# Optimization experiments

Hardware: AMD Instinct MI355X
Metric: run time of the kernel (lower is better)

The kernel has to match this reference:

```python
import jax, jax.numpy as jnp
import numpy as np
import math

D_MODEL = 1024
N_HEADS = 16
D_FF = 4096
KERNEL = 25
EPS = 1e-5


def setup_inputs() -> dict:
    key = jax.random.key(0)
    ks = jax.random.split(key, 16)
    B, L, D = 2, 2048, D_MODEL
    s = 0.02
    inp = {
        'x': jax.random.normal(ks[0], (B, L, D), dtype=jnp.float32),
        'Wq': jax.random.normal(ks[1], (D, D), dtype=jnp.float32) * s,
        'bq': jnp.zeros((D,), jnp.float32),
        'Wk': jax.random.normal(ks[2], (D, D), dtype=jnp.float32) * s,
        'bk': jnp.zeros((D,), jnp.float32),
        'Wv': jax.random.normal(ks[3], (D, D), dtype=jnp.float32) * s,
        'bv': jnp.zeros((D,), jnp.float32),
        'Wo': jax.random.normal(ks[4], (D, D), dtype=jnp.float32) * s,
        'bo': jnp.zeros((D,), jnp.float32),
        'W1': jax.random.normal(ks[5], (D_FF, D), dtype=jnp.float32) * s,
        'b1': jnp.zeros((D_FF,), jnp.float32),
        'W2': jax.random.normal(ks[6], (D, D_FF), dtype=jnp.float32) * s,
        'b2': jnp.zeros((D,), jnp.float32),
        'g1': jnp.ones((D,), jnp.float32),
        'be1': jnp.zeros((D,), jnp.float32),
        'g2': jnp.ones((D,), jnp.float32),
        'be2': jnp.zeros((D,), jnp.float32),
    }
    return inp


def moving_avg(x):
    # torch AvgPool1d(kernel=25, stride=1, padding=12, count_include_pad=True)
    # x: (B, L, D) -> trend: (B, L, D)
    pad = KERNEL // 2
    xp = jnp.pad(x, ((0, 0), (pad, pad), (0, 0)))
    c = jnp.cumsum(xp, axis=1)
    c = jnp.concatenate([jnp.zeros_like(c[:, :1]), c], axis=1)
    return (c[:, KERNEL:] - c[:, :-KERNEL]) / KERNEL


def layernorm(x, g, b):
    mu = jnp.mean(x, axis=-1, keepdims=True)
    var = jnp.mean((x - mu) ** 2, axis=-1, keepdims=True)
    return (x - mu) * jax.lax.rsqrt(var + EPS) * g + b


def reference(x, Wq, bq, Wk, bk, Wv, bv, Wo, bo, W1, b1, W2, b2, g1, be1, g2, be2):
    B, L, D = x.shape
    H, dk = N_HEADS, D // N_HEADS
    # projections (torch Linear: y = x @ W.T + b)
    q = (x @ Wq.T + bq).reshape(B, L, H, dk).transpose(0, 2, 1, 3)
    k = (x @ Wk.T + bk).reshape(B, L, H, dk).transpose(0, 2, 1, 3)
    v = (x @ Wv.T + bv).reshape(B, L, H, dk).transpose(0, 2, 1, 3)
    scores = jnp.einsum('bhld,bhmd->bhlm', q, k) / math.sqrt(dk)
    t = jnp.arange(L, dtype=jnp.float32)
    time_bias = -0.1 * jnp.abs(t[None, :] - t[:, None])  # (L, L)
    attn = jax.nn.softmax(scores + time_bias[None, None], axis=-1)
    ao = jnp.einsum('bhlm,bhmd->bhld', attn, v)
    ao = ao.transpose(0, 2, 1, 3).reshape(B, L, D)
    attn_out = ao @ Wo.T + bo
    x = x + attn_out
    x = moving_avg(x)  # trend kept (x, _ = decomp1(x))
    x = layernorm(x, g1, be1)
    ff = jax.nn.gelu(x @ W1.T + b1, approximate=False) @ W2.T + b2
    x = x + ff
    x = moving_avg(x)  # trend kept again
    x = layernorm(x, g2, be2)
    return x
```

## Files before the change

### kernel.cpp

```cpp
#include <hip/hip_runtime.h>
#include <hip/hip_bf16.h>
#include <math.h>

#define DMODEL 1024
#define LSEQ   2048
#define BATCH  2
#define NHEADS 16
#define DHEAD  64
#define DFF    4096
#define MROWS  (BATCH*LSEQ)

typedef __attribute__((ext_vector_type(8))) short short8;
typedef __attribute__((ext_vector_type(4))) float f32x4;
using bf16 = __hip_bfloat16;

static __device__ __forceinline__ f32x4 mfma16(short8 a, short8 b, f32x4 c) {
    return __builtin_amdgcn_mfma_f32_16x16x32_bf16(a, b, c, 0, 0, 0);
}

static __device__ __forceinline__ void gload16(const void* g, void* l) {
    __builtin_amdgcn_global_load_lds(
        (const __attribute__((address_space(1))) char*)g,
        (__attribute__((address_space(3))) char*)l, 16, 0, 0);
}

static __device__ __forceinline__ bf16 b16(float v) { return __float2bfloat16(v); }

__global__ void f2b1_kernel(const float* __restrict__ in, bf16* __restrict__ out, int n4) {
    int i = blockIdx.x * blockDim.x + threadIdx.x;
    if (i >= n4) return;
    float4 v = reinterpret_cast<const float4*>(in)[i];
    union { ushort4 u; bf16 h[4]; } o;
    o.h[0] = b16(v.x); o.h[1] = b16(v.y); o.h[2] = b16(v.z); o.h[3] = b16(v.w);
    reinterpret_cast<ushort4*>(out)[i] = o.u;
}

__global__ void f2b4_kernel(const float* p0, const float* p1, const float* p2, const float* p3,
                            bf16* o0, bf16* o1, bf16* o2, bf16* o3, int n4) {
    const float* in; bf16* out;
    switch (blockIdx.y) {
        case 0: in = p0; out = o0; break;
        case 1: in = p1; out = o1; break;
        case 2: in = p2; out = o2; break;
        default: in = p3; out = o3; break;
    }
    int i = blockIdx.x * blockDim.x + threadIdx.x;
    if (i >= n4) return;
    float4 v = reinterpret_cast<const float4*>(in)[i];
    union { ushort4 u; bf16 h[4]; } o;
    o.h[0] = b16(v.x); o.h[1] = b16(v.y); o.h[2] = b16(v.z); o.h[3] = b16(v.w);
    reinterpret_cast<ushort4*>(out)[i] = o.u;
}

__global__ void concat3_kernel(const float* __restrict__ a, const float* __restrict__ b,
                               const float* __restrict__ c, float* __restrict__ o) {
    int i = blockIdx.x * blockDim.x + threadIdx.x;
    if (i < DMODEL) { o[i] = a[i]; o[DMODEL + i] = b[i]; o[2 * DMODEL + i] = c[i]; }
}

template<int S>
__global__ __launch_bounds__(256) void reduce_kernel(const float* __restrict__ res,
                                                     const float* __restrict__ P,
                                                     const float* __restrict__ bias,
                                                     float* __restrict__ out, int n4) {
    int i = blockIdx.x * blockDim.x + threadIdx.x;
    if (i >= n4) return;
    float4 acc = reinterpret_cast<const float4*>(res)[i];
#pragma unroll
    for (int s = 0; s < S; ++s) {
        float4 p = reinterpret_cast<const float4*>(P)[i + (size_t)s * (MROWS * DMODEL / 4)];
        acc.x += p.x; acc.y += p.y; acc.z += p.z; acc.w += p.w;
    }
    float4 bs = reinterpret_cast<const float4*>(bias)[i & (DMODEL / 4 - 1)];
    acc.x += bs.x; acc.y += bs.y; acc.z += bs.z; acc.w += bs.w;
    reinterpret_cast<float4*>(out)[i] = acc;
}

template<int EPI>
__global__ __launch_bounds__(256) void gemm_bt(const bf16* __restrict__ A,
                                               const bf16* __restrict__ W,
                                               const float* __restrict__ bias,
                                               void* __restrict__ Cout,
                                               int M, int N, int lda, int ldw, int K) {
    __shared__ bf16 sm[16384];
    const int t    = threadIdx.x;
    const int m0   = blockIdx.x * 128;
    const int n0   = blockIdx.y * 128;
    const int sk   = blockIdx.z;
    const int wave = t >> 6, lane = t & 63;
    const int wr   = (wave >> 1) * 64;
    const int wc   = (wave & 1) * 64;
    const int lr   = lane & 15, lkb = lane >> 4;
    const int srow = t >> 2, scol = (t & 3) * 8;

    const bf16* Ag0 = A + (size_t)(m0 + srow) * lda + (size_t)sk * K + scol;
    const bf16* Ag1 = A + (size_t)(m0 + 64 + srow) * lda + (size_t)sk * K + scol;
    const bf16* Wg0 = W + (size_t)(n0 + srow) * ldw + (size_t)sk * K + scol;
    const bf16* Wg1 = W + (size_t)(n0 + 64 + srow) * ldw + (size_t)sk * K + scol;

    f32x4 acc[4][4];
#pragma unroll
    for (int i = 0; i < 4; ++i)
#pragma unroll
        for (int j = 0; j < 4; ++j)
            acc[i][j] = (f32x4){0.f, 0.f, 0.f, 0.f};

    const int nt = K >> 5;
    auto stage = [&](int buf, int kt) {
        const int off = kt * 32;
        bf16* AsW = sm + buf * 4096 + wave * 512;
        bf16* WsW = sm + 8192 + buf * 4096 + wave * 512;
        gload16(Ag0 + off, AsW);
        gload16(Ag1 + off, AsW + 2048);
        gload16(Wg0 + off, WsW);
        gload16(Wg1 + off, WsW + 2048);
    };

    stage(0, 0);
    __syncthreads();
    int cur = 0;
    for (int kt = 0; kt < nt; ++kt) {
        if (kt + 1 < nt) stage(cur ^ 1, kt + 1);
        short8 a[4], b[4];
#pragma unroll
        for (int i = 0; i < 4; ++i)
            a[i] = *reinterpret_cast<const short8*>(
                &sm[cur * 4096 + (wr + i * 16 + lr) * 32 + lkb * 8]);
#pragma unroll
        for (int j = 0; j < 4; ++j)
            b[j] = *reinterpret_cast<const short8*>(
                &sm[8192 + cur * 4096 + (wc + j * 16 + lr) * 32 + lkb * 8]);
#pragma unroll
        for (int i = 0; i < 4; ++i)
#pragma unroll
            for (int j = 0; j < 4; ++j)
                acc[i][j] = mfma16(b[j], a[i], acc[i][j]);
        __syncthreads();
        cur ^= 1;
    }

    float* Cp = (float*)Cout + (EPI == 3 ? (size_t)sk * M * N : 0);
#pragma unroll
    for (int i = 0; i < 4; ++i) {
        const int row = m0 + wr + i * 16 + lr;
#pragma unroll
        for (int j = 0; j < 4; ++j) {
            const int col = n0 + wc + j * 16 + lkb * 4;
            f32x4 v = acc[i][j];
            if (EPI != 3) {
                float4 bs = *reinterpret_cast<const float4*>(&bias[col]);
                v[0] += bs.x; v[1] += bs.y; v[2] += bs.z; v[3] += bs.w;
            }
            if (EPI == 0 || EPI == 3) {
                float4 ov; ov.x = v[0]; ov.y = v[1]; ov.z = v[2]; ov.w = v[3];
                *reinterpret_cast<float4*>(&Cp[(size_t)row * N + col]) = ov;
            } else if (EPI == 1) {
                union { ushort4 u; bf16 h[4]; } ob;
#pragma unroll
                for (int q = 0; q < 4; ++q) {
                    float x = v[q];
                    float u2 = x * (1.5957691216f + 0.0713548162f * x * x);
                    float e = __expf(fminf(u2, 60.f));
                    ob.h[q] = b16(x * (e / (e + 1.f)));
                }
                *reinterpret_cast<ushort4*>(
                    &reinterpret_cast<bf16*>(Cout)[(size_t)row * N + col]) = ob.u;
            } else {
                union { ushort4 u; bf16 h[4]; } ob;
#pragma unroll
                for (int q = 0; q < 4; ++q) ob.h[q] = b16(v[q]);
                *reinterpret_cast<ushort4*>(
                    &reinterpret_cast<bf16*>(Cout)[(size_t)row * N + col]) = ob.u;
            }
        }
    }
}

__global__ __launch_bounds__(256) void attn_kernel(const bf16* __restrict__ Q,
                                                   const bf16* __restrict__ Km,
                                                   const bf16* __restrict__ V,
                                                   bf16* __restrict__ O,
                                                   int ldq, int ldo) {
    __shared__ bf16 Qs[64][72];
    __shared__ bf16 Ks[64][72];
    __shared__ bf16 VsT[64][72];
    __shared__ bf16 Ps[64][72];
    const int t    = threadIdx.x;
    const int wave = t >> 6, lane = t & 63;
    const int lr   = lane & 15, lkb = lane >> 4;
    const int qt   = blockIdx.x;
    const int q0   = qt * 64;
    const int b    = blockIdx.y >> 4, h = blockIdx.y & 15;
    const size_t base  = (size_t)b * LSEQ * ldq + (size_t)h * DHEAD;
    const size_t baseo = (size_t)b * LSEQ * ldo + (size_t)h * DHEAD;

#pragma unroll
    for (int p = 0; p < 2; ++p) {
        int idx = t + p * 256;
        int row = idx >> 3, c = (idx & 7) * 8;
        *reinterpret_cast<uint4*>(&Qs[row][c]) =
            *reinterpret_cast<const uint4*>(&Q[base + (size_t)(q0 + row) * ldq + c]);
    }
    __syncthreads();
    short8 qa[2];
    qa[0] = *reinterpret_cast<const short8*>(&Qs[wave * 16 + lr][lkb * 8]);
    qa[1] = *reinterpret_cast<const short8*>(&Qs[wave * 16 + lr][32 + lkb * 8]);

    f32x4 o[4];
#pragma unroll
    for (int dj = 0; dj < 4; ++dj) o[dj] = (f32x4){0.f, 0.f, 0.f, 0.f};
    float mrun[4], lrun[4];
#pragma unroll
    for (int q = 0; q < 4; ++q) { mrun[q] = -1e30f; lrun[q] = 0.f; }

    int kt0 = qt - 3; if (kt0 < 0) kt0 = 0;
    int kt1 = qt + 3; if (kt1 > LSEQ / 64 - 1) kt1 = LSEQ / 64 - 1;

    for (int kt = kt0; kt <= kt1; ++kt) {
        const int k0 = kt * 64;
        __syncthreads();
#pragma unroll
        for (int p = 0; p < 2; ++p) {
            int idx = t + p * 256;
            int row = idx >> 3, c = (idx & 7) * 8;
            *reinterpret_cast<uint4*>(&Ks[row][c]) =
                *reinterpret_cast<const uint4*>(&Km[base + (size_t)(k0 + row) * ldq + c]);
        }
        {
            const int vl = lane, vw = wave;
#pragma unroll
            for (int p = 0; p < 2; ++p) {
                int c = vw * 8 + p * 32;
                union { uint4 u; bf16 hh[8]; } tv;
                tv.u = *reinterpret_cast<const uint4*>(&V[base + (size_t)(k0 + vl) * ldq + c]);
#pragma unroll
                for (int e = 0; e < 8; ++e) VsT[c + e][vl] = tv.hh[e];
            }
        }
        __syncthreads();

        f32x4 s[4];
#pragma unroll
        for (int j = 0; j < 4; ++j) {
            short8 kb0 = *reinterpret_cast<const short8*>(&Ks[j * 16 + lr][lkb * 8]);
            short8 kb1 = *reinterpret_cast<const short8*>(&Ks[j * 16 + lr][32 + lkb * 8]);
            f32x4 z = (f32x4){0.f, 0.f, 0.f, 0.f};
            z = mfma16(qa[0], kb0, z);
            z = mfma16(qa[1], kb1, z);
            s[j] = z;
        }
        float mx[4];
#pragma unroll
        for (int q = 0; q < 4; ++q) mx[q] = -1e30f;
#pragma unroll
        for (int j = 0; j < 4; ++j) {
            int cm = k0 + j * 16 + lr;
#pragma unroll
            for (int q = 0; q < 4; ++q) {
                int rq = q0 + wave * 16 + lkb * 4 + q;
                float sv = s[j][q] * 0.125f - 0.1f * fabsf((float)(rq - cm));
                s[j][q] = sv;
                mx[q] = fmaxf(mx[q], sv);
            }
        }
#pragma unroll
        for (int q = 0; q < 4; ++q) {
#pragma unroll
            for (int off = 1; off < 16; off <<= 1)
                mx[q] = fmaxf(mx[q], __shfl_xor(mx[q], off));
        }
        float alpha[4];
#pragma unroll
        for (int q = 0; q < 4; ++q) {
            float mnew = fmaxf(mrun[q], mx[q]);
            alpha[q] = __expf(mrun[q] - mnew);
            mrun[q] = mnew;
        }
        float rs[4] = {0.f, 0.f, 0.f, 0.f};
#pragma unroll
        for (int j = 0; j < 4; ++j) {
#pragma unroll
            for (int q = 0; q < 4; ++q) {
                float p = __expf(s[j][q] - mrun[q]);
                rs[q] += p;
                Ps[wave * 16 + lkb * 4 + q][j * 16 + lr] = b16(p);
            }
        }
#pragma unroll
        for (int q = 0; q < 4; ++q) {
#pragma unroll
            for (int off = 1; off < 16; off <<= 1)
                rs[q] += __shfl_xor(rs[q], off);
            lrun[q] = lrun[q] * alpha[q] + rs[q];
        }
#pragma unroll
        for (int dj = 0; dj < 4; ++dj)
#pragma unroll
            for (int q = 0; q < 4; ++q) o[dj][q] *= alpha[q];

        short8 pa0 = *reinterpret_cast<const short8*>(&Ps[wave * 16 + lr][lkb * 8]);
        short8 pa1 = *reinterpret_cast<const short8*>(&Ps[wave * 16 + lr][32 + lkb * 8]);
#pragma unroll
        for (int dj = 0; dj < 4; ++dj) {
            short8 vb0 = *reinterpret_cast<const short8*>(&VsT[dj * 16 + lr][lkb * 8]);
            short8 vb1 = *reinterpret_cast<const short8*>(&VsT[dj * 16 + lr][32 + lkb * 8]);
            o[dj] = mfma16(pa0, vb0, o[dj]);
            o[dj] = mfma16(pa1, vb1, o[dj]);
        }
    }

#pragma unroll
    for (int dj = 0; dj < 4; ++dj) {
#pragma unroll
        for (int q = 0; q < 4; ++q) {
            int row = q0 + wave * 16 + lkb * 4 + q;
            int col = dj * 16 + lr;
            float val = o[dj][q] / lrun[q];
            O[baseo + (size_t)row * ldo + col] = b16(val);
        }
    }
}

__global__ __launch_bounds__(256) void mavg_ln_kernel(const float* __restrict__ r,
                                                      const float* __restrict__ g,
                                                      const float* __restrict__ be,
                                                      float* __restrict__ out,
                                                      bf16* __restrict__ outb) {
    const int row = (blockIdx.x & 7) * (MROWS / 8) + (blockIdx.x >> 3);
    const int b = row >> 11, l = row & 2047;
    const int t = threadIdx.x, c = t * 4;
    const float* base = r + (size_t)b * LSEQ * DMODEL;
    int j0 = l - 12; if (j0 < 0) j0 = 0;
    int j1 = l + 12; if (j1 > LSEQ - 1) j1 = LSEQ - 1;
    float s0 = 0.f, s1 = 0.f, s2 = 0.f, s3 = 0.f;
    for (int j = j0; j <= j1; ++j) {
        float4 v = *reinterpret_cast<const float4*>(&base[(size_t)j * DMODEL + c]);
        s0 += v.x; s1 += v.y; s2 += v.z; s3 += v.w;
    }
    const float kinv = 1.0f / 25.0f;
    float t0 = s0 * kinv, t1 = s1 * kinv, t2 = s2 * kinv, t3 = s3 * kinv;
    float p1 = t0 + t1 + t2 + t3;
    float p2 = t0 * t0 + t1 * t1 + t2 * t2 + t3 * t3;
    const int lane = t & 63, wv = t >> 6;
#pragma unroll
    for (int off = 1; off < 64; off <<= 1) {
        p1 += __shfl_xor(p1, off);
        p2 += __shfl_xor(p2, off);
    }
    __shared__ float red[8];
    if (lane == 0) { red[wv] = p1; red[4 + wv] = p2; }
    __syncthreads();
    p1 = red[0] + red[1] + red[2] + red[3];
    p2 = red[4] + red[5] + red[6] + red[7];
    const float mu  = p1 * (1.0f / 1024.0f);
    const float var = p2 * (1.0f / 1024.0f) - mu * mu;
    const float inv = rsqrtf(var + 1e-5f);
    float4 gg = *reinterpret_cast<const float4*>(&g[c]);
    float4 bb = *reinterpret_cast<const float4*>(&be[c]);
    float o0 = (t0 - mu) * inv * gg.x + bb.x;
    float o1 = (t1 - mu) * inv * gg.y + bb.y;
    float o2 = (t2 - mu) * inv * gg.z + bb.z;
    float o3 = (t3 - mu) * inv * gg.w + bb.w;
    float4 ov; ov.x = o0; ov.y = o1; ov.z = o2; ov.w = o3;
    *reinterpret_cast<float4*>(&out[(size_t)row * DMODEL + c]) = ov;
    if (outb) {
        union { ushort4 u; bf16 hh[4]; } ob;
        ob.hh[0] = b16(o0); ob.hh[1] = b16(o1); ob.hh[2] = b16(o2); ob.hh[3] = b16(o3);
        reinterpret_cast<ushort4*>(outb + (size_t)row * DMODEL)[t] = ob.u;
    }
}

extern "C" void kernel_launch(void* const* d_in, const int* in_sizes, int n_in,
                              void* d_out, int out_size, void* d_ws, size_t ws_size,
                              hipStream_t stream) {
    const float* x   = (const float*)d_in[0];
    const float* Wq  = (const float*)d_in[1];
    const float* bq  = (const float*)d_in[2];
    const float* Wk  = (const float*)d_in[3];
    const float* bk  = (const float*)d_in[4];
    const float* Wv  = (const float*)d_in[5];
    const float* bv  = (const float*)d_in[6];
    const float* Wo  = (const float*)d_in[7];
    const float* bo  = (const float*)d_in[8];
    const float* W1  = (const float*)d_in[9];
    const float* b1  = (const float*)d_in[10];
    const float* W2  = (const float*)d_in[11];
    const float* b2  = (const float*)d_in[12];
    const float* g1  = (const float*)d_in[13];
    const float* be1 = (const float*)d_in[14];
    const float* g2  = (const float*)d_in[15];
    const float* be2 = (const float*)d_in[16];
    float* out = (float*)d_out;
    char* ws = (char*)d_ws;
    const size_t MB = 1u << 20;

    float* rr   = (float*)(ws + 0);
    bf16* xb    = (bf16*)(ws + 0);
    bf16* qkvb  = (bf16*)(ws + 16 * MB);
    bf16* ab    = (bf16*)(ws + 16 * MB);
    bf16* hb    = (bf16*)(ws + 24 * MB);
    bf16* aob   = (bf16*)(ws + 40 * MB);
    bf16* Wqkvb = (bf16*)(ws + 48 * MB);
    bf16* Wob   = (bf16*)(ws + 54 * MB);
    bf16* W1b   = (bf16*)(ws + 56 * MB);
    bf16* W2b   = (bf16*)(ws + 64 * MB);
    float* P    = (float*)(ws + 72 * MB);
    float* a    = (float*)(ws + 136 * MB);
    float* bqkv = (float*)(ws + 136 * MB);

    f2b1_kernel<<<(MROWS * DMODEL / 4) / 256, 256, 0, stream>>>(x, xb, MROWS * DMODEL / 4);
    f2b4_kernel<<<dim3((DMODEL * DMODEL / 4) / 256, 4), 256, 0, stream>>>(
        Wq, Wk, Wv, Wo,
        Wqkvb, Wqkvb + DMODEL * DMODEL, Wqkvb + 2 * DMODEL * DMODEL, Wob,
        DMODEL * DMODEL / 4);
    f2b4_kernel<<<dim3((DFF * DMODEL / 4) / 256, 2), 256, 0, stream>>>(
        W1, W2, nullptr, nullptr, W1b, W2b, nullptr, nullptr, DFF * DMODEL / 4);
    concat3_kernel<<<4, 256, 0, stream>>>(bq, bk, bv, bqkv);

    dim3 blk(256);
    gemm_bt<2><<<dim3(32, 24), blk, 0, stream>>>(xb, Wqkvb, bqkv, qkvb,
                                                 MROWS, 3 * DMODEL, DMODEL, DMODEL, DMODEL);
    attn_kernel<<<dim3(32, 32), blk, 0, stream>>>(qkvb, qkvb + DMODEL, qkvb + 2 * DMODEL,
                                                  aob, 3 * DMODEL, DMODEL);
    gemm_bt<3><<<dim3(32, 8, 2), blk, 0, stream>>>(aob, Wob, nullptr, P,
                                                   MROWS, DMODEL, DMODEL, DMODEL, DMODEL / 2);
    reduce_kernel<2><<<(MROWS * DMODEL / 4) / 256, blk, 0, stream>>>(x, P, bo, rr, MROWS * DMODEL / 4);
    mavg_ln_kernel<<<MROWS, blk, 0, stream>>>(rr, g1, be1, a, ab);
    gemm_bt<1><<<dim3(32, 32), blk, 0, stream>>>(ab, W1b, b1, hb,
                                                 MROWS, DFF, DMODEL, DMODEL, DMODEL);
    gemm_bt<3><<<dim3(32, 8, 4), blk, 0, stream>>>(hb, W2b, nullptr, P,
                                                   MROWS, DMODEL, DFF, DFF, DFF / 4);
    reduce_kernel<4><<<(MROWS * DMODEL / 4) / 256, blk, 0, stream>>>(a, P, b2, rr, MROWS * DMODEL / 4);
    mavg_ln_kernel<<<MROWS, blk, 0, stream>>>(rr, g2, be2, out, nullptr);
}
```

Measured before the change: 284.8 us.

## Replace 128x128 GEMM with 256x256 tiled, triple-buffered, swizzled-LDS kernel

New measurement: 285.8 us. About the same (+0.4%).

```diff
diff --git a/kernel.cpp b/kernel.cpp
--- a/kernel.cpp
+++ b/kernel.cpp
@@ -77,75 +77,109 @@
 }
 
 template<int EPI>
-__global__ __launch_bounds__(256) void gemm_bt(const bf16* __restrict__ A,
-                                               const bf16* __restrict__ W,
-                                               const float* __restrict__ bias,
-                                               void* __restrict__ Cout,
-                                               int M, int N, int lda, int ldw, int K) {
-    __shared__ bf16 sm[16384];
+__global__ __launch_bounds__(512, 2) void gemm256(const bf16* __restrict__ A,
+                                                  const bf16* __restrict__ W,
+                                                  const float* __restrict__ bias,
+                                                  void* __restrict__ Cout,
+                                                  int M, int N, int lda, int ldw,
+                                                  int K, int nn) {
+    __shared__ bf16 sm[49152];
     const int t    = threadIdx.x;
-    const int m0   = blockIdx.x * 128;
-    const int n0   = blockIdx.y * 128;
+    const int wave = t >> 6, lane = t & 63;
+    const int lr   = lane & 15, lkb = lane >> 4;
+    const int wm   = wave >> 2, wn = wave & 3;
     const int sk   = blockIdx.z;
-    const int wave = t >> 6, lane = t & 63;
-    const int wr   = (wave >> 1) * 64;
-    const int wc   = (wave & 1) * 64;
-    const int lr   = lane & 15, lkb = lane >> 4;
-    const int srow = t >> 2, scol = (t & 3) * 8;
-
-    const bf16* Ag0 = A + (size_t)(m0 + srow) * lda + (size_t)sk * K + scol;
-    const bf16* Ag1 = A + (size_t)(m0 + 64 + srow) * lda + (size_t)sk * K + scol;
-    const bf16* Wg0 = W + (size_t)(n0 + srow) * ldw + (size_t)sk * K + scol;
-    const bf16* Wg1 = W + (size_t)(n0 + 64 + srow) * ldw + (size_t)sk * K + scol;
-
-    f32x4 acc[4][4];
-#pragma unroll
-    for (int i = 0; i < 4; ++i)
+
+    const int nwg = gridDim.x;
+    const int bid = blockIdx.x;
+    const int wg  = (bid & 7) * (nwg >> 3) + (bid >> 3);
+    const int m0  = (wg / nn) * 256;
+    const int n0  = (wg % nn) * 256;
+
+    const bf16* src[4];
+    int dbase[4];
+#pragma unroll
+    for (int u = 0; u < 4; ++u) {
+        const int q  = t + (u & 1) * 512;
+        const int R  = q >> 3;
+        const int ss = (q & 7) ^ (R & 7);
+        const int rp = ss >> 2, c = (ss & 3) * 8;
+        if (u < 2) src[u] = A + (size_t)(m0 + 2 * R + rp) * lda + (size_t)sk * K + c;
+        else       src[u] = W + (size_t)(n0 + 2 * R + rp) * ldw + (size_t)sk * K + c;
+        dbase[u] = ((u >> 1) ? 16384 : 0) + (wave * 64 + (u & 1) * 512) * 16;
+    }
+    char* smb = (char*)sm;
+
+    int aoff[8], boff[4];
+#pragma unroll
+    for (int i = 0; i < 8; ++i) {
+        const int r = wm * 128 + i * 16 + lr, R = r >> 1;
+        aoff[i] = R * 128 + ((((r & 1) << 2) | lkb) ^ (R & 7)) * 16;
+    }
+#pragma unroll
+    for (int j = 0; j < 4; ++j) {
+        const int r = wn * 64 + j * 16 + lr, R = r >> 1;
+        boff[j] = 16384 + R * 128 + ((((r & 1) << 2) | lkb) ^ (R & 7)) * 16;
+    }
+
+    f32x4 acc[8][4];
+#pragma unroll
+    for (int i = 0; i < 8; ++i)
 #pragma unroll
         for (int j = 0; j < 4; ++j)
             acc[i][j] = (f32x4){0.f, 0.f, 0.f, 0.f};
 
     const int nt = K >> 5;
-    auto stage = [&](int buf, int kt) {
-        const int off = kt * 32;
-        bf16* AsW = sm + buf * 4096 + wave * 512;
-        bf16* WsW = sm + 8192 + buf * 4096 + wave * 512;
-        gload16(Ag0 + off, AsW);
-        gload16(Ag1 + off, AsW + 2048);
-        gload16(Wg0 + off, WsW);
-        gload16(Wg1 + off, WsW + 2048);
+    auto STAGE = [&](int bufoff, int kt) {
+        const int koff = kt * 32;
+#pragma unroll
+        for (int u = 0; u < 4; ++u)
+            gload16(src[u] + koff, smb + bufoff + dbase[u]);
     };
 
-    stage(0, 0);
-    __syncthreads();
-    int cur = 0;
+    STAGE(0, 0);
+    if (nt > 1) STAGE(32768, 1);
+    __builtin_amdgcn_sched_barrier(0);
+    if (nt > 1) asm volatile("s_waitcnt vmcnt(4)" ::: "memory");
+    else        asm volatile("s_waitcnt vmcnt(0)" ::: "memory");
+    __builtin_amdgcn_s_barrier();
+    __builtin_amdgcn_sched_barrier(0);
+
+    int curoff = 0, stgoff = 65536;
     for (int kt = 0; kt < nt; ++kt) {
-        if (kt + 1 < nt) stage(cur ^ 1, kt + 1);
-        short8 a[4], b[4];
-#pragma unroll
-        for (int i = 0; i < 4; ++i)
-            a[i] = *reinterpret_cast<const short8*>(
-                &sm[cur * 4096 + (wr + i * 16 + lr) * 32 + lkb * 8]);
+        if (kt + 2 < nt) {
+            STAGE(stgoff, kt + 2);
+            stgoff = (stgoff == 65536) ? 0 : stgoff + 32768;
+        }
+        short8 a[8], b[4];
+#pragma unroll
+        for (int i = 0; i < 8; ++i)
+            a[i] = *reinterpret_cast<const short8*>(smb + curoff + aoff[i]);
 #pragma unroll
         for (int j = 0; j < 4; ++j)
-            b[j] = *reinterpret_cast<const short8*>(
-                &sm[8192 + cur * 4096 + (wc + j * 16 + lr) * 32 + lkb * 8]);
-#pragma unroll
-        for (int i = 0; i < 4; ++i)
+            b[j] = *reinterpret_cast<const short8*>(smb + curoff + boff[j]);
+#pragma unroll
+        for (int i = 0; i < 8; ++i)
 #pragma unroll
             for (int j = 0; j < 4; ++j)
                 acc[i][j] = mfma16(b[j], a[i], acc[i][j]);
-        __syncthreads();
-        cur ^= 1;
+        if (kt + 1 < nt) {
+            __builtin_amdgcn_sched_barrier(0);
+            if (kt + 2 < nt) asm volatile("s_waitcnt vmcnt(4)" ::: "memory");
+            else             asm volatile("s_waitcnt vmcnt(0)" ::: "memory");
+            __builtin_amdgcn_s_barrier();
+            __builtin_amdgcn_sched_barrier(0);
+        }
+        curoff = (curoff == 65536) ? 0 : curoff + 32768;
     }
 
     float* Cp = (float*)Cout + (EPI == 3 ? (size_t)sk * M * N : 0);
 #pragma unroll
-    for (int i = 0; i < 4; ++i) {
-        const int row = m0 + wr + i * 16 + lr;
+    for (int i = 0; i < 8; ++i) {
+        const int row = m0 + wm * 128 + i * 16 + lr;
 #pragma unroll
         for (int j = 0; j < 4; ++j) {
-            const int col = n0 + wc + j * 16 + lkb * 4;
+            const int col = n0 + wn * 64 + j * 16 + lkb * 4;
             f32x4 v = acc[i][j];
             if (EPI != 3) {
                 float4 bs = *reinterpret_cast<const float4*>(&bias[col]);
@@ -417,19 +451,18 @@
         W1, W2, nullptr, nullptr, W1b, W2b, nullptr, nullptr, DFF * DMODEL / 4);
     concat3_kernel<<<4, 256, 0, stream>>>(bq, bk, bv, bqkv);
 
-    dim3 blk(256);
-    gemm_bt<2><<<dim3(32, 24), blk, 0, stream>>>(xb, Wqkvb, bqkv, qkvb,
-                                                 MROWS, 3 * DMODEL, DMODEL, DMODEL, DMODEL);
-    attn_kernel<<<dim3(32, 32), blk, 0, stream>>>(qkvb, qkvb + DMODEL, qkvb + 2 * DMODEL,
+    gemm256<2><<<dim3(192, 1, 1), 512, 0, stream>>>(xb, Wqkvb, bqkv, qkvb,
+                                                    MROWS, 3 * DMODEL, DMODEL, DMODEL, DMODEL, 12);
+    attn_kernel<<<dim3(32, 32), 256, 0, stream>>>(qkvb, qkvb + DMODEL, qkvb + 2 * DMODEL,
                                                   aob, 3 * DMODEL, DMODEL);
-    gemm_bt<3><<<dim3(32, 8, 2), blk, 0, stream>>>(aob, Wob, nullptr, P,
-                                                   MROWS, DMODEL, DMODEL, DMODEL, DMODEL / 2);
-    reduce_kernel<2><<<(MROWS * DMODEL / 4) / 256, blk, 0, stream>>>(x, P, bo, rr, MROWS * DMODEL / 4);
-    mavg_ln_kernel<<<MROWS, blk, 0, stream>>>(rr, g1, be1, a, ab);
-    gemm_bt<1><<<dim3(32, 32), blk, 0, stream>>>(ab, W1b, b1, hb,
-                                                 MROWS, DFF, DMODEL, DMODEL, DMODEL);
-    gemm_bt<3><<<dim3(32, 8, 4), blk, 0, stream>>>(hb, W2b, nullptr, P,
-                                                   MROWS, DMODEL, DFF, DFF, DFF / 4);
-    reduce_kernel<4><<<(MROWS * DMODEL / 4) / 256, blk, 0, stream>>>(a, P, b2, rr, MROWS * DMODEL / 4);
-    mavg_ln_kernel<<<MROWS, blk, 0, stream>>>(rr, g2, be2, out, nullptr);
-}
+    gemm256<3><<<dim3(64, 1, 4), 512, 0, stream>>>(aob, Wob, nullptr, P,
+                                                   MROWS, DMODEL, DMODEL, DMODEL, DMODEL / 4, 4);
+    reduce_kernel<4><<<(MROWS * DMODEL / 4) / 256, 256, 0, stream>>>(x, P, bo, rr, MROWS * DMODEL / 4);
+    mavg_ln_kernel<<<MROWS, 256, 0, stream>>>(rr, g1, be1, a, ab);
+    gemm256<1><<<dim3(256, 1, 1), 512, 0, stream>>>(ab, W1b, b1, hb,
+                                                    MROWS, DFF, DMODEL, DMODEL, DMODEL, 16);
+    gemm256<3><<<dim3(64, 1, 4), 512, 0, stream>>>(hb, W2b, nullptr, P,
+                                                   MROWS, DMODEL, DFF, DFF, DFF / 4, 4);
+    reduce_kernel<4><<<(MROWS * DMODEL / 4) / 256, 256, 0, stream>>>(a, P, b2, rr, MROWS * DMODEL / 4);
+    mavg_ln_kernel<<<MROWS, 256, 0, stream>>>(rr, g2, be2, out, nullptr);
+}
```
